# Optimization experiments

Measured on AMD Instinct MI355X. Metric: run time of the kernel, lower is better.

The kernel has to match this reference:

```python
import jax, jax.numpy as jnp
import numpy as np

C = 256          # C_in == C_out
G = C // 4       # groups = C_in/4 -> 4 channels per group
K = 3
STRIDE = 1
PAD = 2
DIL = 2
EPS = 1e-5

@jax.custom_vjp
def binarize(x):
    # 1-bit sign binarization with straight-through estimator (STE)
    return jnp.sign(x)

def _bin_fwd(x):
    return jnp.sign(x), x

def _bin_bwd(x, g):
    # STE with hardtanh clip: pass grad where |x| <= 1
    return (g * (jnp.abs(x) <= 1.0).astype(g.dtype),)

binarize.defvjp(_bin_fwd, _bin_bwd)

def setup_inputs() -> dict:
    key = jax.random.key(0)
    k1, k2, k3, k4, k5, k6 = jax.random.split(key, 6)
    x = jax.random.normal(k1, (64, C, 32, 32), jnp.float32)
    # grouped conv weight: [C_out, C_in/groups, K, K] = [256, 4, 3, 3]
    weight = jax.random.normal(k2, (C, C // G, K, K), jnp.float32) * 0.1
    gamma = 1.0 + 0.1 * jax.random.normal(k3, (C,), jnp.float32)
    beta = 0.1 * jax.random.normal(k4, (C,), jnp.float32)
    running_mean = 0.1 * jax.random.normal(k5, (C,), jnp.float32)
    running_var = jax.random.uniform(k6, (C,), jnp.float32, 0.5, 1.5)
    return {"x": x, "weight": weight, "gamma": gamma, "beta": beta,
            "running_mean": running_mean, "running_var": running_var}

def reference(x, weight, gamma, beta, running_mean, running_var):
    # BatchNorm2d (inference form with running stats)
    inv = gamma * jax.lax.rsqrt(running_var + EPS)            # [C]
    h = x * inv[None, :, None, None] + (beta - running_mean * inv)[None, :, None, None]
    # binarize activations and weights (1w1a)
    a = binarize(h)
    w = binarize(weight)
    # grouped dilated conv, stride 1, pad 2, dilation 2 -> same HxW
    out = jax.lax.conv_general_dilated(
        a, w,
        window_strides=(STRIDE, STRIDE),
        padding=[(PAD, PAD), (PAD, PAD)],
        rhs_dilation=(DIL, DIL),
        dimension_numbers=("NCHW", "OIHW", "NCHW"),
        feature_group_count=G)
    # channel shuffle: [N,C,H,W] -> [N,g,C/g,H,W] -> [N,C/g,g,H,W] -> [N,C,H,W]
    N, Cc, H, W = out.shape
    out = out.reshape(N, G, Cc // G, H, W).transpose(0, 2, 1, 3, 4).reshape(N, Cc, H, W)
    # identity shortcut (stride == 1)
    return out + x
```

## Files before the change

kernel.cpp:

```cpp
#include <hip/hip_runtime.h>

#ifndef __has_builtin
#define __has_builtin(x) 0
#endif

#if __has_builtin(__builtin_amdgcn_sdot4)
#define DOT4(a, b, c) __builtin_amdgcn_sdot4((a), (b), (c), false)
#else
__device__ __forceinline__ int dot4_sw(int a, int b, int c) {
#pragma unroll
    for (int k = 0; k < 4; ++k)
        c += (int)(signed char)((a >> (8 * k)) & 0xff) *
             (int)(signed char)((b >> (8 * k)) & 0xff);
    return c;
}
#define DOT4(a, b, c) dot4_sw((a), (b), (c))
#endif

constexpr int CH   = 256;
constexpr int NPIX = 1024;
constexpr float BN_EPS = 1e-5f;

__global__ __launch_bounds__(256, 4)
void bconv(const float* __restrict__ x,
           const float* __restrict__ wgt,
           const float* __restrict__ gamma,
           const float* __restrict__ beta,
           const float* __restrict__ rmean,
           const float* __restrict__ rvar,
           float* __restrict__ out) {
    const int tid  = threadIdx.x;
    const int n0   = (blockIdx.x >> 6) * 2;
    const int g    = blockIdx.x & 63;
    const int pix0 = tid * 4;
    const int row  = pix0 >> 5;
    const int col0 = pix0 & 31;
    const float* xnA = x + n0 * CH * NPIX;
    const float* xnB = xnA + CH * NPIX;
    float* onA = out + n0 * CH * NPIX;
    float* onB = onA + CH * NPIX;

    float4 xvA[3][4];
#pragma unroll
    for (int kh = 0; kh < 3; ++kh) {
        const int rsc = min(max(row + 2 * kh - 2, 0), 31);
        const float* rp = xnA + g * 4 * NPIX + rsc * 32 + col0;
#pragma unroll
        for (int ci = 0; ci < 4; ++ci)
            xvA[kh][ci] = *(const float4*)(rp + ci * NPIX);
    }
    float4 scA[4];
#pragma unroll
    for (int c2 = 0; c2 < 4; ++c2)
        scA[c2] = *(const float4*)(xnA + (c2 * 64 + g) * NPIX + pix0);

    const int* wb = (const int*)(wgt + g * 144);
    int wq[4][9];
#pragma unroll
    for (int c2 = 0; c2 < 4; ++c2)
#pragma unroll
        for (int t = 0; t < 9; ++t) {
            int pk = 0;
#pragma unroll
            for (int ci = 0; ci < 4; ++ci) {
                const int b = wb[c2 * 36 + ci * 9 + t];
                const int s = ((b & 0x7fffffff) == 0) ? 0 : ((b < 0) ? -1 : 1);
                pk |= (s & 0xff) << (8 * ci);
            }
            wq[c2][t] = pk;
        }

    float inv[4], bias[4];
#pragma unroll
    for (int ci = 0; ci < 4; ++ci) {
        const int c = g * 4 + ci;
        float r  = __fdiv_rn(1.0f, __fsqrt_rn(__fadd_rn(rvar[c], BN_EPS)));
        inv[ci]  = __fmul_rn(gamma[c], r);
        bias[ci] = __fsub_rn(beta[c], __fmul_rn(rmean[c], inv[ci]));
    }

    auto pack = [&](const float4 xv[3][4], int pkc[3][4]) {
#pragma unroll
        for (int kh = 0; kh < 3; ++kh) {
            const bool ok = (unsigned)(row + 2 * kh - 2) < 32u;
#pragma unroll
            for (int p = 0; p < 4; ++p) {
                int v = 0;
#pragma unroll
                for (int ci = 0; ci < 4; ++ci) {
                    float h = __fadd_rn(__fmul_rn(((const float*)&xv[kh][ci])[p], inv[ci]), bias[ci]);
                    int s = (h > 0.f) ? 1 : ((h < 0.f) ? -1 : 0);
                    v |= (s & 0xff) << (8 * ci);
                }
                pkc[kh][p] = ok ? v : 0;
            }
        }
    };

    const bool le = (col0 == 0), re = (col0 == 28);
    auto compute_store = [&](const int pkc[3][4], const float4 sc[4], float* on) {
        int a[3][8];
#pragma unroll
        for (int kh = 0; kh < 3; ++kh) {
            int l2 = __shfl_up(pkc[kh][2], 1);
            int l3 = __shfl_up(pkc[kh][3], 1);
            int r0 = __shfl_down(pkc[kh][0], 1);
            int r1 = __shfl_down(pkc[kh][1], 1);
            a[kh][0] = le ? 0 : l2;
            a[kh][1] = le ? 0 : l3;
            a[kh][2] = pkc[kh][0]; a[kh][3] = pkc[kh][1];
            a[kh][4] = pkc[kh][2]; a[kh][5] = pkc[kh][3];
            a[kh][6] = re ? 0 : r0;
            a[kh][7] = re ? 0 : r1;
        }
#pragma unroll
        for (int c2 = 0; c2 < 4; ++c2) {
            float4 o;
#pragma unroll
            for (int p = 0; p < 4; ++p) {
                int acc = 0;
#pragma unroll
                for (int kh = 0; kh < 3; ++kh)
#pragma unroll
                    for (int kw = 0; kw < 3; ++kw)
                        acc = DOT4(a[kh][p + 2 * kw], wq[c2][kh * 3 + kw], acc);
                ((float*)&o)[p] = __fadd_rn((float)acc, ((const float*)&sc[c2])[p]);
            }
            *(float4*)(on + (c2 * 64 + g) * NPIX + pix0) = o;
        }
    };

    int pkcA[3][4];
    pack(xvA, pkcA);

    float4 xvB[3][4];
#pragma unroll
    for (int kh = 0; kh < 3; ++kh) {
        const int rsc = min(max(row + 2 * kh - 2, 0), 31);
        const float* rp = xnB + g * 4 * NPIX + rsc * 32 + col0;
#pragma unroll
        for (int ci = 0; ci < 4; ++ci)
            xvB[kh][ci] = *(const float4*)(rp + ci * NPIX);
    }

    compute_store(pkcA, scA, onA);

    int pkcB[3][4];
    pack(xvB, pkcB);

    float4 scB[4];
#pragma unroll
    for (int c2 = 0; c2 < 4; ++c2)
        scB[c2] = *(const float4*)(xnB + (c2 * 64 + g) * NPIX + pix0);

    compute_store(pkcB, scB, onB);
}

extern "C" void kernel_launch(void* const* d_in, const int* in_sizes, int n_in,
                              void* d_out, int out_size, void* d_ws, size_t ws_size,
                              hipStream_t stream) {
    const float* x     = (const float*)d_in[0];
    const float* wgt   = (const float*)d_in[1];
    const float* gamma = (const float*)d_in[2];
    const float* beta  = (const float*)d_in[3];
    const float* rmean = (const float*)d_in[4];
    const float* rvar  = (const float*)d_in[5];
    float* out = (float*)d_out;

    const int N = in_sizes[0] / (CH * NPIX);
    bconv<<<(N / 2) * 64, 256, 0, stream>>>(x, wgt, gamma, beta, rmean, rvar, out);
}
```

Baseline: 37.28 us.

## Swizzle block order, fence scheduling for early loads, use nontemporal stores

Block indices are remapped so that consecutive blocks land on different batch/group combinations, which changes which blocks run together and their cache and channel locality. Scheduling barriers pin the issue of global loads, and the second image's shortcut loads now come before its pack step, so memory latency overlaps with compute. Output stores become nontemporal to avoid polluting the cache. The swizzle hard-codes a block count of 2048 (8 × 256), so it only maps blocks correctly when N is 64, and the fences may keep the compiler from interleaving instructions in better ways.

```diff
diff --git a/kernel.cpp b/kernel.cpp
--- a/kernel.cpp
+++ b/kernel.cpp
@@ -17,6 +17,14 @@
 #define DOT4(a, b, c) dot4_sw((a), (b), (c))
 #endif
 
+#if __has_builtin(__builtin_amdgcn_sched_barrier)
+#define SCHED_FENCE() __builtin_amdgcn_sched_barrier(0)
+#else
+#define SCHED_FENCE() asm volatile("" ::: "memory")
+#endif
+
+typedef float vfloat4 __attribute__((ext_vector_type(4)));
+
 constexpr int CH   = 256;
 constexpr int NPIX = 1024;
 constexpr float BN_EPS = 1e-5f;
@@ -29,9 +37,12 @@
            const float* __restrict__ rmean,
            const float* __restrict__ rvar,
            float* __restrict__ out) {
-    const int tid  = threadIdx.x;
-    const int n0   = (blockIdx.x >> 6) * 2;
-    const int g    = blockIdx.x & 63;
+    const int tid = threadIdx.x;
+    const int bid = blockIdx.x;
+    const int swz = (bid & 7) * 256 + (bid >> 3);
+    const int n0  = (swz >> 6) * 2;
+    const int g   = swz & 63;
+
     const int pix0 = tid * 4;
     const int row  = pix0 >> 5;
     const int col0 = pix0 & 31;
@@ -40,19 +51,20 @@
     float* onA = out + n0 * CH * NPIX;
     float* onB = onA + CH * NPIX;
 
-    float4 xvA[3][4];
+    vfloat4 xvA[3][4];
 #pragma unroll
     for (int kh = 0; kh < 3; ++kh) {
         const int rsc = min(max(row + 2 * kh - 2, 0), 31);
         const float* rp = xnA + g * 4 * NPIX + rsc * 32 + col0;
 #pragma unroll
         for (int ci = 0; ci < 4; ++ci)
-            xvA[kh][ci] = *(const float4*)(rp + ci * NPIX);
+            xvA[kh][ci] = *(const vfloat4*)(rp + ci * NPIX);
     }
-    float4 scA[4];
+    vfloat4 scA[4];
 #pragma unroll
     for (int c2 = 0; c2 < 4; ++c2)
-        scA[c2] = *(const float4*)(xnA + (c2 * 64 + g) * NPIX + pix0);
+        scA[c2] = *(const vfloat4*)(xnA + (c2 * 64 + g) * NPIX + pix0);
+    SCHED_FENCE();
 
     const int* wb = (const int*)(wgt + g * 144);
     int wq[4][9];
@@ -79,7 +91,7 @@
         bias[ci] = __fsub_rn(beta[c], __fmul_rn(rmean[c], inv[ci]));
     }
 
-    auto pack = [&](const float4 xv[3][4], int pkc[3][4]) {
+    auto pack = [&](const vfloat4 xv[3][4], int pkc[3][4]) {
 #pragma unroll
         for (int kh = 0; kh < 3; ++kh) {
             const bool ok = (unsigned)(row + 2 * kh - 2) < 32u;
@@ -88,7 +100,7 @@
                 int v = 0;
 #pragma unroll
                 for (int ci = 0; ci < 4; ++ci) {
-                    float h = __fadd_rn(__fmul_rn(((const float*)&xv[kh][ci])[p], inv[ci]), bias[ci]);
+                    float h = __fadd_rn(__fmul_rn(xv[kh][ci][p], inv[ci]), bias[ci]);
                     int s = (h > 0.f) ? 1 : ((h < 0.f) ? -1 : 0);
                     v |= (s & 0xff) << (8 * ci);
                 }
@@ -98,7 +110,7 @@
     };
 
     const bool le = (col0 == 0), re = (col0 == 28);
-    auto compute_store = [&](const int pkc[3][4], const float4 sc[4], float* on) {
+    auto compute_store = [&](const int pkc[3][4], const vfloat4 sc[4], float* on) {
         int a[3][8];
 #pragma unroll
         for (int kh = 0; kh < 3; ++kh) {
@@ -115,7 +127,7 @@
         }
 #pragma unroll
         for (int c2 = 0; c2 < 4; ++c2) {
-            float4 o;
+            vfloat4 o;
 #pragma unroll
             for (int p = 0; p < 4; ++p) {
                 int acc = 0;
@@ -124,35 +136,36 @@
 #pragma unroll
                     for (int kw = 0; kw < 3; ++kw)
                         acc = DOT4(a[kh][p + 2 * kw], wq[c2][kh * 3 + kw], acc);
-                ((float*)&o)[p] = __fadd_rn((float)acc, ((const float*)&sc[c2])[p]);
+                o[p] = __fadd_rn((float)acc, sc[c2][p]);
             }
-            *(float4*)(on + (c2 * 64 + g) * NPIX + pix0) = o;
+            __builtin_nontemporal_store(o, (vfloat4*)(on + (c2 * 64 + g) * NPIX + pix0));
         }
     };
 
     int pkcA[3][4];
     pack(xvA, pkcA);
 
-    float4 xvB[3][4];
+    vfloat4 xvB[3][4];
 #pragma unroll
     for (int kh = 0; kh < 3; ++kh) {
         const int rsc = min(max(row + 2 * kh - 2, 0), 31);
         const float* rp = xnB + g * 4 * NPIX + rsc * 32 + col0;
 #pragma unroll
         for (int ci = 0; ci < 4; ++ci)
-            xvB[kh][ci] = *(const float4*)(rp + ci * NPIX);
+            xvB[kh][ci] = *(const vfloat4*)(rp + ci * NPIX);
     }
+    SCHED_FENCE();
 
     compute_store(pkcA, scA, onA);
 
+    vfloat4 scB[4];
+#pragma unroll
+    for (int c2 = 0; c2 < 4; ++c2)
+        scB[c2] = *(const vfloat4*)(xnB + (c2 * 64 + g) * NPIX + pix0);
+    SCHED_FENCE();
+
     int pkcB[3][4];
     pack(xvB, pkcB);
-
-    float4 scB[4];
-#pragma unroll
-    for (int c2 = 0; c2 < 4; ++c2)
-        scB[c2] = *(const float4*)(xnB + (c2 * 64 + g) * NPIX + pix0);
-
     compute_store(pkcB, scB, onB);
 }
 
```

Result: faster. 30.52 us, median of 2 (-18.1%).
